# Kernel tuning notes

Hardware: AMD Instinct MI355X
Metric: run time of the kernel (lower is better)

## Reference

```python
import jax, jax.numpy as jnp
import numpy as np

K_INIT = 16  # self.k from __init__

def setup_inputs() -> dict:
    key = jax.random.key(0)
    center = jax.random.normal(key, (8192, 64), dtype=jnp.float32)
    return {"center": center}

def _cdist(x):
    # Euclidean pairwise distances, matmul-based like torch.cdist(p=2).
    x2 = jnp.sum(x * x, axis=-1)  # [N]
    d2 = x2[:, None] + x2[None, :] - 2.0 * (x @ x.T)  # [N, N]
    d2 = jnp.maximum(d2, 0.0)
    # safe sqrt (grad-safe at 0; forward identical)
    d = jnp.sqrt(jnp.where(d2 > 0.0, d2, 1.0))
    return jnp.where(d2 > 0.0, d, 0.0)

def reference(center):
    n, d_feat = center.shape
    k = min(K_INIT + 1, d_feat)  # faithful to torch: min(self.k + 1, center.shape[1])
    dist = _cdist(center)  # [N, N]
    # smallest-k via top_k on negated distances
    _, indices = jax.lax.top_k(-dist, k)  # [N, k]
    neighbor_indices = indices[:, 1:]  # drop self, [N, k-1]
    mean_dists = jnp.take_along_axis(dist, neighbor_indices, axis=1).mean(axis=1)  # [N]
    logp = jax.nn.log_softmax(mean_dists, axis=0)  # = softmax(mean_dists).log()
    q = 1.0 / n
    # F.kl_div(p.log(), q, reduction='sum') = sum q * (log q - log p)
    loss = jnp.sum(q * (jnp.log(jnp.float32(q)) - logp))
    return loss
```

## Files before the change

kernel.cpp:

```cpp
#include <hip/hip_runtime.h>
#include <hip/hip_bf16.h>
#include <math.h>

#define N_PTS 8192
#define D_FEAT 64
#define TPB 1024
#define ROWS_B 32
#define PASSES 16
#define CAP 512
#define NORM_OFF 0
#define MIN_OFF  8192
#define TAU_OFF  9216
#define SV_OFF   9248
#define LDS_F    (9248 + 32 * CAP)

typedef __attribute__((ext_vector_type(8))) short short8v;
typedef __attribute__((ext_vector_type(16))) float f32x16;

__device__ ushort g_X2[N_PTS * D_FEAT];
__device__ float  g_x2n[N_PTS];
__device__ float  g_md[N_PTS];

__global__ __launch_bounds__(256) void pack_kernel(const float* __restrict__ x) {
    const int row = blockIdx.x * 256 + threadIdx.x;
    const int chunk = row >> 5, r = row & 31;
    const float4* xr = (const float4*)(x + (size_t)row * D_FEAT);
    ushort* base = g_X2 + (size_t)chunk * 2048 + r * 8;
    float norm = 0.f;
    #pragma unroll
    for (int it = 0; it < 8; ++it) {
        float4 a = xr[2 * it], b = xr[2 * it + 1];
        float vals[8] = {a.x, a.y, a.z, a.w, b.x, b.y, b.z, b.w};
        uint hi[8];
        #pragma unroll
        for (int e = 0; e < 8; ++e) {
            float v = vals[e];
            norm += v * v;
            uint u = __float_as_uint(v);
            hi[e] = (u + 0x7fffu + ((u >> 16) & 1u)) >> 16;
        }
        *(uint4*)(base + it * 256) = make_uint4(
            hi[0] | (hi[1] << 16), hi[2] | (hi[3] << 16),
            hi[4] | (hi[5] << 16), hi[6] | (hi[7] << 16));
    }
    g_x2n[row] = norm;
}

#define CE(A, B) { float lo_ = fminf(A, B); float hi_ = fmaxf(A, B); A = lo_; B = hi_; }

__global__ __launch_bounds__(TPB, 4) void nn_kernel() {
    __shared__ float s_mem[LDS_F];
    __shared__ int   s_cnt[32];
    const int t    = threadIdx.x;
    const int lane = t & 63;
    const int w    = t >> 6;
    const int il   = lane & 31;
    const int h    = lane >> 5;
    const int ib   = blockIdx.x;
    const int i0   = ib * ROWS_B;
    const float INF = __builtin_inff();

    {
        float4* s4 = (float4*)s_mem;
        const float4* g4 = (const float4*)g_x2n;
        #pragma unroll
        for (int q = 0; q < 2; ++q) s4[t + q * TPB] = g4[t + q * TPB];
        if (t < 32) s_cnt[t] = 0;
    }

    const short8v* Xf = (const short8v*)g_X2;

    short8v bfr[4];
    {
        const short8v* bp = Xf + ((size_t)ib * 8 + h) * 32 + il;
        #pragma unroll
        for (int tt = 0; tt < 4; ++tt) bfr[tt] = bp[tt * 64];
    }
    __syncthreads();

    const short8v* abase = Xf + ((size_t)w * 8 + h) * 32 + il;
    #define ALOAD(dst, p) { \
        const short8v* ab_ = abase + (size_t)(p) * 4096; \
        _Pragma("unroll") \
        for (int tt = 0; tt < 4; ++tt) dst[tt] = ab_[tt * 64]; }

    #define MFMA4(accv, areg) { \
        _Pragma("unroll") \
        for (int r = 0; r < 16; ++r) accv[r] = 0.f; \
        _Pragma("unroll") \
        for (int tt = 0; tt < 4; ++tt) \
            accv = __builtin_amdgcn_mfma_f32_32x32x16_bf16(areg[tt], bfr[tt], accv, 0, 0, 0); }

    float mmin = INF;
    #define EPILOG_MIN(accv, p) { \
        const int cl_ = (p) * 16 + w; \
        _Pragma("unroll") \
        for (int g = 0; g < 4; ++g) { \
            float4 xq = *(const float4*)&s_mem[cl_ * 32 + 8 * g + 4 * h]; \
            float cand[4] = {xq.x, xq.y, xq.z, xq.w}; \
            _Pragma("unroll") \
            for (int e = 0; e < 4; ++e) \
                mmin = fminf(mmin, fmaf(-2.f, accv[4 * g + e], cand[e])); \
        } }

    {
        short8v a0[4], a1[4];
        f32x16 acc;
        ALOAD(a0, 0);
        #pragma unroll 1
        for (int pp = 0; pp < PASSES / 2; ++pp) {
            const int p0 = 2 * pp, p1 = 2 * pp + 1;
            ALOAD(a1, p1);
            MFMA4(acc, a0);
            EPILOG_MIN(acc, p0);
            if (pp < PASSES / 2 - 1) ALOAD(a0, p0 + 2);
            MFMA4(acc, a1);
            EPILOG_MIN(acc, p1);
        }
    }
    s_mem[MIN_OFF + il * 32 + (w * 2 + h)] = mmin;
    __syncthreads();

    {
        const int r2 = 2 * w + (lane >> 5);
        const int idx = lane & 31;
        float m = s_mem[MIN_OFF + r2 * 32 + idx];
        #pragma unroll
        for (int k = 2; k <= 32; k <<= 1) {
            #pragma unroll
            for (int j = k >> 1; j > 0; j >>= 1) {
                float o = __shfl_xor(m, j);
                const bool low = ((idx & j) == 0);
                const bool up  = ((idx & k) == 0);
                float mn = fminf(m, o), mx = fmaxf(m, o);
                m = (low == up) ? mn : mx;
            }
        }
        if (idx == 16) s_mem[TAU_OFF + r2] = m;
    }
    __syncthreads();

    const float mytau = s_mem[TAU_OFF + il];
    #define EPILOG_FLT(accv, p) { \
        const int cl_ = (p) * 16 + w; \
        _Pragma("unroll") \
        for (int g = 0; g < 4; ++g) { \
            float4 xq = *(const float4*)&s_mem[cl_ * 32 + 8 * g + 4 * h]; \
            float cand[4] = {xq.x, xq.y, xq.z, xq.w}; \
            _Pragma("unroll") \
            for (int e = 0; e < 4; ++e) { \
                float v = fmaf(-2.f, accv[4 * g + e], cand[e]); \
                if (v <= mytau) { \
                    int ix_ = atomicAdd(&s_cnt[il], 1); \
                    if (ix_ < CAP) s_mem[SV_OFF + il * CAP + ix_] = v; \
                } \
            } \
        } }

    {
        short8v a0[4], a1[4];
        f32x16 acc;
        ALOAD(a0, 0);
        #pragma unroll 1
        for (int pp = 0; pp < PASSES / 2; ++pp) {
            const int p0 = 2 * pp, p1 = 2 * pp + 1;
            ALOAD(a1, p1);
            MFMA4(acc, a0);
            EPILOG_FLT(acc, p0);
            if (pp < PASSES / 2 - 1) ALOAD(a0, p0 + 2);
            MFMA4(acc, a1);
            EPILOG_FLT(acc, p1);
        }
    }
    __syncthreads();

    {
        const int r2 = 2 * w + (lane >> 5);
        const int sl = lane & 31;
        const int row = i0 + r2;
        int n = s_cnt[r2];
        if (n > CAP) n = CAP;
        float tl[16];
        #pragma unroll
        for (int q = 0; q < 16; ++q) {
            const int ix = sl + 32 * q;
            tl[q] = (ix < n) ? s_mem[SV_OFF + r2 * CAP + ix] : INF;
        }
        CE(tl[0],tl[8]) CE(tl[1],tl[9]) CE(tl[2],tl[10]) CE(tl[3],tl[11])
        CE(tl[4],tl[12]) CE(tl[5],tl[13]) CE(tl[6],tl[14]) CE(tl[7],tl[15])
        CE(tl[0],tl[4]) CE(tl[1],tl[5]) CE(tl[2],tl[6]) CE(tl[3],tl[7])
        CE(tl[8],tl[12]) CE(tl[9],tl[13]) CE(tl[10],tl[14]) CE(tl[11],tl[15])
        CE(tl[4],tl[8]) CE(tl[5],tl[9]) CE(tl[6],tl[10]) CE(tl[7],tl[11])
        CE(tl[0],tl[2]) CE(tl[1],tl[3]) CE(tl[4],tl[6]) CE(tl[5],tl[7])
        CE(tl[8],tl[10]) CE(tl[9],tl[11]) CE(tl[12],tl[14]) CE(tl[13],tl[15])
        CE(tl[2],tl[8]) CE(tl[3],tl[9]) CE(tl[6],tl[12]) CE(tl[7],tl[13])
        CE(tl[2],tl[4]) CE(tl[3],tl[5]) CE(tl[6],tl[8]) CE(tl[7],tl[9])
        CE(tl[10],tl[12]) CE(tl[11],tl[13])
        CE(tl[0],tl[1]) CE(tl[2],tl[3]) CE(tl[4],tl[5]) CE(tl[6],tl[7])
        CE(tl[8],tl[9]) CE(tl[10],tl[11]) CE(tl[12],tl[13]) CE(tl[14],tl[15])
        CE(tl[1],tl[8]) CE(tl[3],tl[10]) CE(tl[5],tl[12]) CE(tl[7],tl[14])
        CE(tl[1],tl[4]) CE(tl[3],tl[6]) CE(tl[5],tl[8]) CE(tl[7],tl[10])
        CE(tl[9],tl[12]) CE(tl[11],tl[14])
        CE(tl[1],tl[2]) CE(tl[3],tl[4]) CE(tl[5],tl[6]) CE(tl[7],tl[8])
        CE(tl[9],tl[10]) CE(tl[11],tl[12]) CE(tl[13],tl[14])

        const float x2r = g_x2n[row];
        float sum = 0.f;
        #pragma unroll 1
        for (int it = 0; it < 17; ++it) {
            float m = tl[0]; int src = sl;
            #pragma unroll
            for (int off = 16; off > 0; off >>= 1) {
                float om = __shfl_xor(m, off);
                int os = __shfl_xor(src, off);
                if (om < m || (om == m && os < src)) { m = om; src = os; }
            }
            if (it > 0) sum += sqrtf(fmaxf(m + x2r, 0.f));
            const bool pop = (sl == src);
            #pragma unroll
            for (int k = 0; k < 15; ++k) tl[k] = pop ? tl[k + 1] : tl[k];
            tl[15] = pop ? INF : tl[15];
        }
        if (sl == 0) g_md[row] = sum * (1.f / 16.f);
    }
}

__global__ __launch_bounds__(1024) void loss_kernel(float* __restrict__ out) {
    __shared__ float s[1024];
    const int t = threadIdx.x;

    float m = -__builtin_inff();
    for (int j = t; j < N_PTS; j += 1024) m = fmaxf(m, g_md[j]);
    s[t] = m; __syncthreads();
    for (int off = 512; off > 0; off >>= 1) {
        if (t < off) s[t] = fmaxf(s[t], s[t + off]);
        __syncthreads();
    }
    m = s[0]; __syncthreads();

    float se = 0.f, sm = 0.f;
    for (int j = t; j < N_PTS; j += 1024) {
        float v = g_md[j];
        se += expf(v - m);
        sm += v;
    }
    s[t] = se; __syncthreads();
    for (int off = 512; off > 0; off >>= 1) {
        if (t < off) s[t] += s[t + off];
        __syncthreads();
    }
    float S = s[0]; __syncthreads();
    s[t] = sm; __syncthreads();
    for (int off = 512; off > 0; off >>= 1) {
        if (t < off) s[t] += s[t + off];
        __syncthreads();
    }
    float M = s[0];

    if (t == 0) {
        const float n = (float)N_PTS;
        out[0] = -logf(n) - M / n + (m + logf(S));
    }
}

extern "C" void kernel_launch(void* const* d_in, const int* in_sizes, int n_in,
                              void* d_out, int out_size, void* d_ws, size_t ws_size,
                              hipStream_t stream) {
    const float* x = (const float*)d_in[0];
    float* out = (float*)d_out;

    pack_kernel<<<N_PTS / 256, 256, 0, stream>>>(x);
    nn_kernel<<<N_PTS / ROWS_B, TPB, 0, stream>>>();
    loss_kernel<<<1, 1024, 0, stream>>>(out);
}
```

Baseline: 56.57 us.

## Fuse pack, kNN and loss kernels into one cooperative kernel with grid syncs

Merges the three separate launches (bf16 packing plus norms, nearest-neighbour search, log-softmax loss) into a single cooperative kernel, using grid-wide syncs between stages. The packing is redistributed so each block packs its own 32 rows, with the norm reduced through shuffles. The aim is to remove two kernel launch gaps. In exchange it adds two grid barriers, has block 0 run the loss serially while the rest of the grid idles, and changes launch bounds from 4 to 1, which may alter register allocation.

```diff
diff --git a/kernel.cpp b/kernel.cpp
--- a/kernel.cpp
+++ b/kernel.cpp
@@ -1,10 +1,14 @@
 #include <hip/hip_runtime.h>
 #include <hip/hip_bf16.h>
+#include <hip/hip_cooperative_groups.h>
 #include <math.h>
+
+namespace cg = cooperative_groups;
 
 #define N_PTS 8192
 #define D_FEAT 64
 #define TPB 1024
+#define GRID 256
 #define ROWS_B 32
 #define PASSES 16
 #define CAP 512
@@ -21,34 +25,10 @@
 __device__ float  g_x2n[N_PTS];
 __device__ float  g_md[N_PTS];
 
-__global__ __launch_bounds__(256) void pack_kernel(const float* __restrict__ x) {
-    const int row = blockIdx.x * 256 + threadIdx.x;
-    const int chunk = row >> 5, r = row & 31;
-    const float4* xr = (const float4*)(x + (size_t)row * D_FEAT);
-    ushort* base = g_X2 + (size_t)chunk * 2048 + r * 8;
-    float norm = 0.f;
-    #pragma unroll
-    for (int it = 0; it < 8; ++it) {
-        float4 a = xr[2 * it], b = xr[2 * it + 1];
-        float vals[8] = {a.x, a.y, a.z, a.w, b.x, b.y, b.z, b.w};
-        uint hi[8];
-        #pragma unroll
-        for (int e = 0; e < 8; ++e) {
-            float v = vals[e];
-            norm += v * v;
-            uint u = __float_as_uint(v);
-            hi[e] = (u + 0x7fffu + ((u >> 16) & 1u)) >> 16;
-        }
-        *(uint4*)(base + it * 256) = make_uint4(
-            hi[0] | (hi[1] << 16), hi[2] | (hi[3] << 16),
-            hi[4] | (hi[5] << 16), hi[6] | (hi[7] << 16));
-    }
-    g_x2n[row] = norm;
-}
-
 #define CE(A, B) { float lo_ = fminf(A, B); float hi_ = fmaxf(A, B); A = lo_; B = hi_; }
 
-__global__ __launch_bounds__(TPB, 4) void nn_kernel() {
+__global__ __launch_bounds__(TPB, 1) void fused_kernel(
+    const float* __restrict__ x, float* __restrict__ out) {
     __shared__ float s_mem[LDS_F];
     __shared__ int   s_cnt[32];
     const int t    = threadIdx.x;
@@ -59,6 +39,32 @@
     const int ib   = blockIdx.x;
     const int i0   = ib * ROWS_B;
     const float INF = __builtin_inff();
+    cg::grid_group grid = cg::this_grid();
+
+    if (t < 256) {
+        const int r = t >> 3, u = t & 7;
+        const int row = i0 + r;
+        const float4* xr = (const float4*)(x + (size_t)row * D_FEAT + u * 8);
+        float4 a = xr[0], b = xr[1];
+        float vals[8] = {a.x, a.y, a.z, a.w, b.x, b.y, b.z, b.w};
+        float norm = 0.f;
+        uint hi[8];
+        #pragma unroll
+        for (int e = 0; e < 8; ++e) {
+            float v = vals[e];
+            norm += v * v;
+            uint uu = __float_as_uint(v);
+            hi[e] = (uu + 0x7fffu + ((uu >> 16) & 1u)) >> 16;
+        }
+        *(uint4*)(g_X2 + ((size_t)ib * 8 + u) * 256 + r * 8) = make_uint4(
+            hi[0] | (hi[1] << 16), hi[2] | (hi[3] << 16),
+            hi[4] | (hi[5] << 16), hi[6] | (hi[7] << 16));
+        norm += __shfl_xor(norm, 1);
+        norm += __shfl_xor(norm, 2);
+        norm += __shfl_xor(norm, 4);
+        if (u == 0) g_x2n[row] = norm;
+    }
+    grid.sync();
 
     {
         float4* s4 = (float4*)s_mem;
@@ -223,43 +229,43 @@
         }
         if (sl == 0) g_md[row] = sum * (1.f / 16.f);
     }
-}
-
-__global__ __launch_bounds__(1024) void loss_kernel(float* __restrict__ out) {
-    __shared__ float s[1024];
-    const int t = threadIdx.x;
-
-    float m = -__builtin_inff();
-    for (int j = t; j < N_PTS; j += 1024) m = fmaxf(m, g_md[j]);
-    s[t] = m; __syncthreads();
-    for (int off = 512; off > 0; off >>= 1) {
-        if (t < off) s[t] = fmaxf(s[t], s[t + off]);
-        __syncthreads();
-    }
-    m = s[0]; __syncthreads();
-
-    float se = 0.f, sm = 0.f;
-    for (int j = t; j < N_PTS; j += 1024) {
-        float v = g_md[j];
-        se += expf(v - m);
-        sm += v;
-    }
-    s[t] = se; __syncthreads();
-    for (int off = 512; off > 0; off >>= 1) {
-        if (t < off) s[t] += s[t + off];
-        __syncthreads();
-    }
-    float S = s[0]; __syncthreads();
-    s[t] = sm; __syncthreads();
-    for (int off = 512; off > 0; off >>= 1) {
-        if (t < off) s[t] += s[t + off];
-        __syncthreads();
-    }
-    float M = s[0];
-
-    if (t == 0) {
-        const float n = (float)N_PTS;
-        out[0] = -logf(n) - M / n + (m + logf(S));
+
+    grid.sync();
+
+    if (ib == 0) {
+        float* s = s_mem;
+        float m = -INF;
+        for (int j = t; j < N_PTS; j += TPB) m = fmaxf(m, g_md[j]);
+        s[t] = m; __syncthreads();
+        for (int off = 512; off > 0; off >>= 1) {
+            if (t < off) s[t] = fmaxf(s[t], s[t + off]);
+            __syncthreads();
+        }
+        m = s[0]; __syncthreads();
+
+        float se = 0.f, sm = 0.f;
+        for (int j = t; j < N_PTS; j += TPB) {
+            float v = g_md[j];
+            se += expf(v - m);
+            sm += v;
+        }
+        s[t] = se; __syncthreads();
+        for (int off = 512; off > 0; off >>= 1) {
+            if (t < off) s[t] += s[t + off];
+            __syncthreads();
+        }
+        float S = s[0]; __syncthreads();
+        s[t] = sm; __syncthreads();
+        for (int off = 512; off > 0; off >>= 1) {
+            if (t < off) s[t] += s[t + off];
+            __syncthreads();
+        }
+        float M = s[0];
+
+        if (t == 0) {
+            const float n = (float)N_PTS;
+            out[0] = -logf(n) - M / n + (m + logf(S));
+        }
     }
 }
 
@@ -269,7 +275,7 @@
     const float* x = (const float*)d_in[0];
     float* out = (float*)d_out;
 
-    pack_kernel<<<N_PTS / 256, 256, 0, stream>>>(x);
-    nn_kernel<<<N_PTS / ROWS_B, TPB, 0, stream>>>();
-    loss_kernel<<<1, 1024, 0, stream>>>(out);
+    void* kargs[2] = {(void*)&x, (void*)&out};
+    hipLaunchCooperativeKernel((void*)fused_kernel, dim3(GRID), dim3(TPB),
+                               kargs, 0, stream);
 }
```

Result: slower. 121.7 us (+115.2%).
